# Kernel tuning notes

Hardware: AMD Instinct MI355X
Metric: run time of the kernel (lower is better)

The kernel has to match this reference:

```python
import jax, jax.numpy as jnp
import numpy as np

B, T, D_IN, D_H, F = 64, 512, 128, 512, 32


def setup_inputs() -> dict:
    key = jax.random.key(0)
    ks = jax.random.split(key, 8)
    s_in = 1.0 / np.sqrt(D_IN)
    s_h = 1.0 / np.sqrt(D_H)
    return {
        "input_sequence": jax.random.normal(ks[0], (B, T, D_IN), dtype=jnp.float32),
        "Wx0": jax.random.normal(ks[1], (D_H, D_IN), dtype=jnp.float32) * s_in,
        "b0": jnp.zeros((D_H,), dtype=jnp.float32),
        "Wh0": jax.random.normal(ks[2], (D_H, D_H), dtype=jnp.float32) * (0.8 * s_h),
        "d0": jnp.asarray(0.9, dtype=jnp.float32),
        "Wx1": jax.random.normal(ks[3], (D_H, D_H), dtype=jnp.float32) * s_h,
        "b1": jnp.zeros((D_H,), dtype=jnp.float32),
        "Wh1": jax.random.normal(ks[4], (D_H, D_H), dtype=jnp.float32) * (0.8 * s_h),
        "d1": jnp.asarray(0.9, dtype=jnp.float32),
        "Wp": jax.random.normal(ks[5], (D_IN, D_H), dtype=jnp.float32) * s_h,
        "bp": jnp.zeros((D_IN,), dtype=jnp.float32),
        "forecast_steps": F,
    }


def reference(input_sequence, Wx0, b0, Wh0, d0, Wx1, b1, Wh1, d1, Wp, bp, forecast_steps):
    batch = input_sequence.shape[0]
    hdim = Wh0.shape[0]

    def step(h0, h1, x):
        # h_t = decay * W_h h_{t-1} + W_x x_t + b ; layer 1 consumes updated h0
        h0 = d0 * (h0 @ Wh0.T) + x @ Wx0.T + b0
        h1 = d1 * (h1 @ Wh1.T) + h0 @ Wx1.T + b1
        return h0, h1

    # ---- encode context (scan over time, time-major) ----
    xs = jnp.swapaxes(input_sequence, 0, 1)  # [T, B, D_in]
    h0 = jnp.zeros((batch, hdim), dtype=input_sequence.dtype)
    h1 = jnp.zeros((batch, hdim), dtype=input_sequence.dtype)

    def enc(carry, xt):
        return step(*carry, xt), None

    (h0, h1), _ = jax.lax.scan(enc, (h0, h1), xs)

    pred0 = h1 @ Wp.T + bp  # [B, D_in]

    def dec(carry, _):
        h0, h1, p = carry
        h0, h1 = step(h0, h1, p)
        p_new = h1 @ Wp.T + bp
        return (h0, h1, p_new), p_new

    _, rest = jax.lax.scan(dec, (h0, h1, pred0), None, length=forecast_steps - 1)
    forecasts = jnp.concatenate([pred0[None], rest], axis=0)  # [F, B, D_in]
    return jnp.swapaxes(forecasts, 0, 1)  # [B, F, D_in]
```

## Files before the change

### kernel.cpp

```cpp
#include <hip/hip_runtime.h>
#include <cstddef>


typedef _Float16 f16;
typedef _Float16 f16x8 __attribute__((ext_vector_type(8)));
typedef _Float16 f16x4 __attribute__((ext_vector_type(4)));
typedef float f32x4 __attribute__((ext_vector_type(4)));

#define NCTR 32
#define LDA  136
#define ALPHAF 0.00390625f
#define RALPHAF 256.0f
#define DIN 128
#define NF 32

constexpr int SZ = 512*512;
constexpr int off_cat   = 0;
constexpr int off_catA1 = 327680;
constexpr int off_A0c   = 851968;
constexpr int off_A1c   = 1114112;
constexpr int off_Wpr   = 1376256;
constexpr int off_Wpc   = 1441792;
constexpr int off_Gr    = 1507328;
constexpr int off_Gc    = 2555904;
constexpr int off_P0    = 3604480;
constexpr int off_P1    = 5177344;
constexpr int GPr       = 6750208;
constexpr int GPc       = 7798784;
constexpr int GQr       = 8847360;
constexpr int GQc       = 9895936;
constexpr int off_Xin   = 10944512;
constexpr int BA        = 15138816;
constexpr int BB        = 17235968;
constexpr int BC        = 19333120;
constexpr int BD        = 21430272;
constexpr int off_S     = 23527424;
constexpr int off_Dc    = 25624576;
constexpr int off_Db    = 25690112;
constexpr int off_b0h   = 25952256;
constexpr int off_b1h   = 25952768;
constexpr int off_b0ah  = 25953280;
constexpr int off_b1ah  = 25953792;
constexpr int off_bph   = 25954304;
constexpr int off_bpX   = 25954432;
constexpr int off_ctr   = 25962624;

constexpr int P0r(int s){ return off_P0 + s*524288; }
constexpr int P0c(int s){ return off_P0 + s*524288 + 262144; }
constexpr int P1r(int s){ return off_P1 + s*524288; }
constexpr int P1c(int s){ return off_P1 + s*524288 + 262144; }
constexpr int Bb(int k){ return k==0 ? off_Dc : off_Db + (k-1)*65536; }

struct Op {
  int type;
  int m_off, m_rstride, rows, cols;
  int k1, x1_off, x1_ks, x1_s1, x1_s2;
  int k2, x2_off, x2_ks, x2_s1, x2_s2;
  int add_off, add_ks, add_s1, add_s2;
  int bias_off; float scale;
  int y_off, y_ks, y_s1, y_s2;
  int yt_off, yt_rstride;
  int out32, tile_base;
};
constexpr int MAXOPS = 80, MAXG = 32;
struct Plan { Op ops[MAXOPS]; int gstart[MAXG+1]; int gtiles[MAXG]; int nops, ng; };

constexpr Op mko() {
  Op o{};
  o.type=0; o.m_off=0; o.m_rstride=512; o.rows=512; o.cols=512;
  o.k1=512; o.x1_off=0; o.x1_ks=512; o.x1_s1=64; o.x1_s2=0;
  o.k2=0; o.x2_off=0; o.x2_ks=512; o.x2_s1=64; o.x2_s2=0;
  o.add_off=-1; o.add_ks=512; o.add_s1=64; o.add_s2=0;
  o.bias_off=-1; o.scale=1.0f;
  o.y_off=-1; o.y_ks=512; o.y_s1=64; o.y_s2=0;
  o.yt_off=-1; o.yt_rstride=512; o.out32=0; o.tile_base=0;
  return o;
}
constexpr int op_ntiles(const Op& o){ return (o.rows>>6)*(o.cols>>5); }

struct Builder { Plan p{}; int nops=0, ng=0, gtile=0; };
constexpr void push(Builder& b, Op o){ o.tile_base=b.gtile; b.gtile+=op_ntiles(o); b.p.ops[b.nops++]=o; }
constexpr void endg(Builder& b){ b.p.gtiles[b.ng]=b.gtile; b.ng++; b.p.gstart[b.ng]=b.nops; b.gtile=0; }

constexpr Op SQ2(int m,int mrs,int x1c,int yc,int yr){
  Op o=mko(); o.m_off=m; o.m_rstride=mrs; o.x1_off=x1c; o.y_off=yc; o.yt_off=yr; return o; }
constexpr Op SQG(int mr,int xc,int yc,int yr){
  Op o=mko(); o.rows=1024; o.cols=1024; o.k1=1024; o.m_off=mr; o.m_rstride=1024;
  o.x1_off=xc; o.x1_ks=1024; o.y_off=yc; o.y_ks=1024; o.yt_off=yr; o.yt_rstride=1024; return o; }
constexpr Op P2S(int s){
  Op o=mko(); o.cols=4096; o.bias_off=off_b0h;
  o.k2=128; o.x2_off=off_Xin; o.x2_ks=128; o.x2_s1=512; o.x2_s2=(s-1)*64;
  o.y_off=(s&1)?BA:BB;
  if (s==1){ o.m_off=off_cat+512; o.m_rstride=640; o.k1=0; }
  else { o.m_off=off_cat; o.m_rstride=640; o.k1=512; o.x1_off=(s&1)?BB:BA; }
  return o; }
constexpr Op HS(int s){
  Op o=mko(); o.m_off=off_cat; o.m_rstride=640; o.cols=4096;
  o.k1=512; o.x1_off=(s&1)?BC:BB;
  o.k2=128; o.x2_off=off_Xin; o.x2_ks=128; o.x2_s1=512; o.x2_s2=(s-1)*64;
  o.bias_off=off_b0h; o.y_off=(s&1)?BB:BC; return o; }
constexpr Op RS(int s){
  Op o=mko(); o.cols=4096; o.bias_off=off_b1h;
  if (s==1){ o.m_off=off_catA1+512; o.m_rstride=1024; o.k1=512; o.x1_off=BB; o.y_off=BD; }
  else { o.m_off=off_catA1; o.m_rstride=1024; o.k1=512; o.x1_off=(s&1)?BA:BD;
         o.k2=512; o.x2_off=(s&1)?BB:BC; o.x2_ks=512; o.x2_s1=64; o.x2_s2=0;
         o.y_off=(s&1)?BD:BA; }
  return o; }
constexpr Op SCAN(int m,int d,int inb,int outb){
  Op o=mko(); o.m_off=m; o.cols=4096-d*64; o.x1_off=inb;
  o.add_off=inb; o.add_s2=d*64; o.y_off=outb; o.y_s2=d*64; return o; }
constexpr Op SCOPY(int d,int inb,int outb){
  Op o=mko(); o.k1=0; o.cols=d*64; o.add_off=inb; o.y_off=outb; return o; }
constexpr Op FOLDL(int m,int cols,int inb,int outb){
  Op o=mko(); o.m_off=m; o.cols=cols; o.x1_off=inb; o.x1_s1=128;
  o.add_off=inb; o.add_s1=128; o.add_s2=64; o.y_off=outb; return o; }
constexpr Op DECA(int k,int moff){
  Op o=mko(); int m=1<<k;
  o.rows=1024; o.cols=m*64; o.k1=1024; o.m_off=moff; o.m_rstride=1024;
  o.x1_off=off_S; o.x1_ks=1024; o.bias_off=Bb(k);
  o.y_off=off_S; o.y_ks=1024; o.y_s2=m*64; return o; }
constexpr Op DECB(int k,int moff){
  Op o=mko(); o.rows=1024; o.cols=64; o.k1=1024; o.m_off=moff; o.m_rstride=1024;
  o.x1_off=Bb(k); o.x1_ks=1024; o.bias_off=Bb(k);
  o.y_off=Bb(k+1); o.y_ks=1024; return o; }

constexpr Plan build_plan() {
  Builder b{}; b.p.gstart[0]=0;
  push(b, SQ2(off_cat,640,off_A0c,P0c(0),P0r(0)));
  push(b, SQ2(off_catA1,1024,off_A1c,P1c(0),P1r(0)));
  { Op o=mko(); o.m_off=off_cat+512; o.m_rstride=640; o.k1=128; o.x1_off=off_Wpc; o.x1_ks=128;
    o.y_off=off_Gc+512*1024; o.y_ks=1024; o.yt_off=off_Gr+512; o.yt_rstride=1024; push(b,o); }
  { Op o=mko(); o.m_off=off_cat+512; o.m_rstride=640; o.k1=128; o.x1_off=off_bpX; o.x1_ks=128;
    o.cols=64; o.bias_off=off_b0ah; o.scale=ALPHAF; o.y_off=off_Dc; o.y_ks=1024; push(b,o); }
  push(b, P2S(1)); endg(b);
  push(b, SQ2(P0r(0),512,P0c(0),P0c(1),P0r(1)));
  push(b, SQ2(P1r(0),512,P1c(0),P1c(1),P1r(1)));
  { Op o=mko(); o.m_off=off_catA1+512; o.m_rstride=1024; o.x1_off=off_A0c;
    o.y_off=off_Gc+512; o.y_ks=1024; o.yt_off=off_Gr+512*1024; o.yt_rstride=1024; push(b,o); }
  { Op o=mko(); o.m_off=off_catA1+512; o.m_rstride=1024; o.x1_off=off_Dc; o.x1_ks=1024;
    o.cols=64; o.bias_off=off_b1ah; o.y_off=off_Dc+512; o.y_ks=1024; push(b,o); }
  push(b, P2S(2)); endg(b);
  push(b, SQ2(P0r(1),512,P0c(1),P0c(2),P0r(2)));
  push(b, SQ2(P1r(1),512,P1c(1),P1c(2),P1r(2)));
  { Op o=mko(); o.m_off=off_catA1+512; o.m_rstride=1024; o.x1_off=off_Gc+512*1024; o.x1_ks=1024;
    o.add_off=off_A1c; o.y_off=off_Gc+512*1024+512; o.y_ks=1024;
    o.yt_off=off_Gr+512*1024+512; o.yt_rstride=1024; push(b,o); }
  push(b, P2S(3)); endg(b);
  push(b, SQ2(P0r(2),512,P0c(2),P0c(0),P0r(0)));
  push(b, SQ2(P1r(2),512,P1c(2),P1c(0),P1r(0)));
  push(b, P2S(4)); endg(b);
  push(b, SQ2(P0r(0),512,P0c(0),P0c(1),P0r(1)));
  push(b, SQ2(P1r(0),512,P1c(0),P1c(1),P1r(1)));
  push(b, P2S(5)); endg(b);
  push(b, P2S(6));
  push(b, SQG(off_Gr, off_Gc, GPc, GPr)); endg(b);
  push(b, P2S(7)); endg(b);
  push(b, P2S(8)); endg(b);
  push(b, SCAN(P0r(2), 1, BB, BA)); push(b, SCOPY(1, BB, BA)); endg(b);
  push(b, SCAN(P0r(0), 2, BA, BB)); push(b, SCOPY(2, BA, BB)); endg(b);
  push(b, SCAN(P0r(1), 4, BB, BA)); push(b, SCOPY(4, BB, BA)); endg(b);
  { Op o=mko(); o.m_off=off_cat; o.m_rstride=640; o.cols=4032; o.k1=512; o.x1_off=BA;
    o.k2=128; o.x2_off=off_Xin; o.x2_ks=128; o.x2_s1=512; o.x2_s2=512;
    o.bias_off=off_b0h; o.y_off=BB; o.y_s2=64; push(b,o); }
  { Op o=mko(); o.m_off=off_cat+512; o.m_rstride=640; o.cols=64; o.k1=0;
    o.k2=128; o.x2_off=off_Xin; o.x2_ks=128; o.x2_s1=512; o.x2_s2=0;
    o.bias_off=off_b0h; o.y_off=BB; push(b,o); }
  endg(b);
  for (int s=1; s<=7; ++s){ push(b, HS(s+1)); push(b, RS(s)); endg(b); }
  push(b, RS(8));
  { Op o=mko(); o.k1=0; o.cols=64; o.add_off=BC; o.add_s2=4032; o.scale=ALPHAF;
    o.y_off=off_S; o.y_ks=1024; push(b,o); }
  endg(b);
  push(b, FOLDL(P1r(2), 2048, BA, BB)); endg(b);
  push(b, FOLDL(P1r(0), 1024, BB, BC)); endg(b);
  { Op o=mko(); o.m_off=P1r(1); o.cols=64; o.x1_off=BC; o.x1_s2=896;
    o.add_off=BC; o.add_s2=960; o.scale=ALPHAF;
    o.y_off=off_S+512; o.y_ks=1024; push(b,o); }
  endg(b);
  push(b, DECA(0, off_Gr)); push(b, DECB(0, off_Gr)); endg(b);
  push(b, DECA(1, GPr)); push(b, DECB(1, GPr)); push(b, SQG(GPr,GPc,GQc,GQr)); endg(b);
  push(b, DECA(2, GQr)); push(b, DECB(2, GQr)); push(b, SQG(GQr,GQc,GPc,GPr)); endg(b);
  push(b, DECA(3, GPr)); push(b, DECB(3, GPr)); push(b, SQG(GPr,GPc,GQc,GQr)); endg(b);
  push(b, DECA(4, GQr)); endg(b);
  { Op o=mko(); o.m_off=off_Wpr; o.rows=128; o.cols=2048; o.x1_off=off_S+512; o.x1_ks=1024;
    o.bias_off=off_bph; o.scale=RALPHAF; o.out32=1; push(b,o); }
  endg(b);
  b.p.nops=b.nops; b.p.ng=b.ng;
  return b.p;
}
static constexpr Plan h_plan = build_plan();
__device__ __constant__ Plan d_plan = h_plan;

__device__ inline void issueA4(const f16* p, f16x8 (&r)[4]) {
  asm volatile(
    "global_load_dwordx4 %0, %4, off\n\t"
    "global_load_dwordx4 %1, %4, off offset:16\n\t"
    "global_load_dwordx4 %2, %4, off offset:32\n\t"
    "global_load_dwordx4 %3, %4, off offset:48"
    : "=&v"(r[0]), "=&v"(r[1]), "=&v"(r[2]), "=&v"(r[3])
    : "v"(p) : "memory");
}
__device__ inline void issueB2(const f16* p, f16x8 (&r)[2]) {
  asm volatile(
    "global_load_dwordx4 %0, %2, off\n\t"
    "global_load_dwordx4 %1, %2, off offset:16"
    : "=&v"(r[0]), "=&v"(r[1]) : "v"(p) : "memory");
}
__device__ inline void issue_ld8(const f16* p, f16x4& r) {
  asm volatile("global_load_dwordx2 %0, %1, off"
               : "=&v"(r) : "v"(p) : "memory");
}
__device__ inline void st8_cc(f16* p, f16x4 v) {
  asm volatile("global_store_dwordx2 %0, %1, off sc0 sc1" :: "v"(p), "v"(v) : "memory");
}
__device__ inline void st2_cc(f16* p, f16 v) {
  unsigned d = __builtin_bit_cast(unsigned short, v);
  asm volatile("global_store_short %0, %1, off sc0 sc1" :: "v"(p), "v"(d) : "memory");
}
__device__ inline unsigned ld_u32_cc(const unsigned* p) {
  unsigned r;
  asm volatile("global_load_dword %0, %1, off sc0 sc1\n\ts_waitcnt vmcnt(0)"
               : "=&v"(r) : "v"(p) : "memory");
  return r;
}
__device__ inline void st_u32_cc(unsigned* p, unsigned v) {
  asm volatile("global_store_dword %0, %1, off sc0 sc1" :: "v"(p), "v"(v) : "memory");
}
__device__ inline void l2_inv() {
  asm volatile("buffer_inv sc0 sc1\n\ts_waitcnt vmcnt(0)" ::: "memory");
}

__device__ inline void grid_barrier(unsigned* ctrs, unsigned epoch) {
  __syncthreads();
  if (threadIdx.x == 0)
    __hip_atomic_fetch_add(&ctrs[(blockIdx.x & (NCTR-1))*32], 1u,
                           __ATOMIC_RELAXED, __HIP_MEMORY_SCOPE_AGENT);
  if (blockIdx.x == 0) {
    if (threadIdx.x < NCTR) {
      const unsigned tgt = epoch * (gridDim.x / NCTR);
      while (ld_u32_cc(&ctrs[threadIdx.x*32]) < tgt)
        __builtin_amdgcn_s_sleep(1);
    }
    __syncthreads();
    if (threadIdx.x < NCTR)
      st_u32_cc(&ctrs[(NCTR + threadIdx.x)*32], epoch);
  } else if (threadIdx.x == 0) {
    const unsigned fl = (NCTR + (blockIdx.x & (NCTR-1)))*32;
    while (ld_u32_cc(&ctrs[fl]) < epoch)
      __builtin_amdgcn_s_sleep(1);
  }
  if (threadIdx.x == 0) l2_inv();
  __syncthreads();
}

__device__ inline void chunk_srcs(const Op& o, const f16* w, int r0, int c0, int kc,
                                  const f16*& pa, const f16*& pb) {
  const int tid = threadIdx.x;
  pa = w + o.m_off + (size_t)(r0 + (tid>>2)) * o.m_rstride + kc + (tid&3)*32;
  int C = c0 + (tid>>3);
  int xo, xks, xs1, xs2, xk;
  if (kc < o.k1) { xo=o.x1_off; xks=o.x1_ks; xs1=o.x1_s1; xs2=o.x1_s2; xk=kc; }
  else           { xo=o.x2_off; xks=o.x2_ks; xs1=o.x2_s1; xs2=o.x2_s2; xk=kc-o.k1; }
  int xcol = xs1*(C>>6) + (C&63) + xs2;
  pb = w + xo + (size_t)xcol*xks + xk + (tid&7)*16;
}

__device__ inline void st_lds(f16* lsA, f16* lsB, const f16x8 (&ra)[4], const f16x8 (&rb)[2]) {
  const int tid = threadIdx.x;
  f16* da = lsA + (tid>>2)*LDA + (tid&3)*32;
#pragma unroll
  for (int i=0;i<4;++i) *(f16x8*)(da + i*8) = ra[i];
  f16* db = lsB + (tid>>3)*LDA + (tid&7)*16;
#pragma unroll
  for (int i=0;i<2;++i) *(f16x8*)(db + i*8) = rb[i];
}

__device__ inline void mfma_lds(const f16* lsA, const f16* lsB, f32x4 (&acc)[2]) {
  const int tid = threadIdx.x, lane = tid & 63, wid = tid >> 6;
  const int ko = (lane >> 4) * 8, rl = lane & 15;
#pragma unroll
  for (int kb = 0; kb < 4; ++kb) {
    f16x8 a = *(const f16x8*)(lsA + (wid*16 + rl) * LDA + kb*32 + ko);
#pragma unroll
    for (int n = 0; n < 2; ++n) {
      f16x8 bb = *(const f16x8*)(lsB + (n*16 + rl) * LDA + kb*32 + ko);
      acc[n] = __builtin_amdgcn_mfma_f32_16x16x32_f16(a, bb, acc[n], 0, 0, 0);
    }
  }
}

#define CH_STEP(c_, raX, rbX)                                                  \
  do {                                                                         \
    asm volatile("s_waitcnt lgkmcnt(0)" ::: "memory");                         \
    __builtin_amdgcn_s_barrier();                                              \
    __builtin_amdgcn_sched_barrier(0);                                         \
    int rem_ = nch - 1 - (c_);                                                 \
    if (rem_ >= 2)      asm volatile("s_waitcnt vmcnt(12)" ::: "memory");      \
    else if (rem_ == 1) asm volatile("s_waitcnt vmcnt(6)"  ::: "memory");      \
    else                asm volatile("s_waitcnt vmcnt(0)"  ::: "memory");      \
    __builtin_amdgcn_sched_barrier(0);                                         \
    st_lds(lsA, lsB, raX, rbX);                                                \
    asm volatile("s_waitcnt lgkmcnt(0)" ::: "memory");                         \
    __builtin_amdgcn_s_barrier();                                              \
    __builtin_amdgcn_sched_barrier(0);                                         \
    if ((c_) + 3 < nch) {                                                      \
      chunk_srcs(o, w, r0, c0, ((c_)+3)*128, pa, pb);                          \
      issueA4(pa, raX); issueB2(pb, rbX);                                      \
    }                                                                          \
    mfma_lds(lsA, lsB, acc);                                                   \
  } while (0)

__device__ void run_tile(const Op& o, int local, f16* w, float* out, f16* lsA, f16* lsB) {
  int nct = o.cols >> 5;
  int rg = local / nct, ct = local - rg * nct;
  int r0 = rg << 6, c0 = ct << 5;
  f32x4 acc[2];
  acc[0] = f32x4{0.f,0.f,0.f,0.f}; acc[1] = f32x4{0.f,0.f,0.f,0.f};
  int nch = (o.k1 + o.k2) >> 7;
  if (nch > 0) {
    const f16 *pa, *pb;
    f16x8 ra0[4], rb0[2], ra1[4], rb1[2], ra2[4], rb2[2];
    chunk_srcs(o, w, r0, c0, 0, pa, pb);
    issueA4(pa, ra0); issueB2(pb, rb0);
    if (nch > 1) { chunk_srcs(o, w, r0, c0, 128, pa, pb);
                   issueA4(pa, ra1); issueB2(pb, rb1); }
    if (nch > 2) { chunk_srcs(o, w, r0, c0, 256, pa, pb);
                   issueA4(pa, ra2); issueB2(pb, rb2); }
    for (int c = 0; c < nch; c += 3) {
      CH_STEP(c, ra0, rb0);
      if (c + 1 < nch) CH_STEP(c+1, ra1, rb1);
      if (c + 2 < nch) CH_STEP(c+2, ra2, rb2);
    }
  }
  const int tid = threadIdx.x, lane = tid & 63, wid = tid >> 6;
  const int q4 = (lane >> 4) * 4, cl = lane & 15;
  const int r = r0 + wid*16 + q4;
  f16x4 addv[2], biasv;
  bool pend = false;
  if (o.add_off >= 0) {
#pragma unroll
    for (int n = 0; n < 2; ++n) {
      int C = c0 + n*16 + cl;
      int acol = o.add_s1 * (C>>6) + (C&63) + o.add_s2;
      const f16* ap = w + o.add_off + (size_t)acol * o.add_ks + r;
      issue_ld8(ap, addv[n]); pend = true;
    }
  }
  if (o.bias_off >= 0) {
    const f16* bp2 = w + o.bias_off + r;
    issue_ld8(bp2, biasv); pend = true;
  }
  if (pend) asm volatile("s_waitcnt vmcnt(0)" ::: "memory");
#pragma unroll
  for (int n = 0; n < 2; ++n) {
    int C = c0 + n*16 + cl;
    f32x4 v = acc[n];
    if (o.add_off >= 0) {
      v[0]+=(float)addv[n][0]; v[1]+=(float)addv[n][1];
      v[2]+=(float)addv[n][2]; v[3]+=(float)addv[n][3];
    }
    v[0]*=o.scale; v[1]*=o.scale; v[2]*=o.scale; v[3]*=o.scale;
    if (o.bias_off >= 0) {
      v[0]+=(float)biasv[0]; v[1]+=(float)biasv[1];
      v[2]+=(float)biasv[2]; v[3]+=(float)biasv[3];
    }
    if (o.y_off >= 0) {
      int ycol = o.y_s1 * (C>>6) + (C&63) + o.y_s2;
      f16* yp = w + o.y_off + (size_t)ycol * o.y_ks + r;
      f16x4 h; h[0]=(f16)v[0]; h[1]=(f16)v[1]; h[2]=(f16)v[2]; h[3]=(f16)v[3];
      st8_cc(yp, h);
    }
    if (o.yt_off >= 0) {
      f16* tp = w + o.yt_off;
      st2_cc(tp + (size_t)(r+0)*o.yt_rstride + C, (f16)v[0]);
      st2_cc(tp + (size_t)(r+1)*o.yt_rstride + C, (f16)v[1]);
      st2_cc(tp + (size_t)(r+2)*o.yt_rstride + C, (f16)v[2]);
      st2_cc(tp + (size_t)(r+3)*o.yt_rstride + C, (f16)v[3]);
    }
    if (o.out32) {
      float* op2 = out + (size_t)(C & 63) * (NF*DIN) + (size_t)(C >> 6) * DIN + r;
      op2[0]=v[0]; op2[1]=v[1]; op2[2]=v[2]; op2[3]=v[3];
    }
  }
}

__global__ __launch_bounds__(256, 4) void rnn_main(f16* w, float* out) {
  __shared__ f16 lsA[64*LDA];
  __shared__ f16 lsB[32*LDA];
  unsigned* ctrs = (unsigned*)(w + off_ctr);
  const int wg = blockIdx.x;
  const int stride = gridDim.x;
  const int ng = d_plan.ng;
  for (int g = 0; g < ng; ++g) {
    int o0 = d_plan.gstart[g], o1 = d_plan.gstart[g+1];
    int gtot = d_plan.gtiles[g];
    for (int t = wg; t < gtot; t += stride) {
      int oi = o0;
      while (oi + 1 < o1 && t >= d_plan.ops[oi+1].tile_base) ++oi;
      run_tile(d_plan.ops[oi], t - d_plan.ops[oi].tile_base, w, out, lsA, lsB);
    }
    grid_barrier(ctrs, (unsigned)(g + 1));
  }
}

__global__ void rnn_prep(f16* w, const float* X, const float* Wx0, const float* b0,
    const float* Wh0, const float* d0p, const float* Wx1, const float* b1,
    const float* Wh1, const float* d1p, const float* Wp, const float* bp)
{
  const float d0 = d0p[0], d1 = d1p[0];
  const long n0=512L*640, n1=512L*1024, n2=(long)SZ, n3=(long)SZ, n4=128L*512, n5=512L*128,
             n6=(long)SZ, n7=(long)SZ, n8=32768L*128, n9=512, n10=512, n11=512, n12=512,
             n13=128, n14=64L*128, n15=2048;
  const long total = n0+n1+n2+n3+n4+n5+n6+n7+n8+n9+n10+n11+n12+n13+n14+n15;
  for (long idx = (long)blockIdx.x*blockDim.x + threadIdx.x; idx < total;
       idx += (long)gridDim.x*blockDim.x) {
    long j = idx;
    if (j < n0) { int r=(int)(j/640), c=(int)(j%640);
      w[off_cat+j] = (f16)(c<512 ? d0*Wh0[(long)r*512+c] : Wx0[(long)r*128+(c-512)]); continue; }
    j -= n0;
    if (j < n1) { int r=(int)(j>>10), c=(int)(j&1023);
      w[off_catA1+j] = (f16)(c<512 ? d1*Wh1[(long)r*512+c] : Wx1[(long)r*512+(c-512)]); continue; }
    j -= n1;
    if (j < n2) { int c=(int)(j>>9), r=(int)(j&511); w[off_A0c+j] = (f16)(d0*Wh0[(long)r*512+c]); continue; }
    j -= n2;
    if (j < n3) { int c=(int)(j>>9), r=(int)(j&511); w[off_A1c+j] = (f16)(d1*Wh1[(long)r*512+c]); continue; }
    j -= n3;
    if (j < n4) { w[off_Wpr+j] = (f16)Wp[j]; continue; }
    j -= n4;
    if (j < n5) { int c=(int)(j>>7), k=(int)(j&127); w[off_Wpc+j] = (f16)Wp[(long)k*512+c]; continue; }
    j -= n5;
    if (j < n6) { int r=(int)(j>>9), c=(int)(j&511);
      w[off_Gr + (long)r*1024 + c] = (f16)(d0*Wh0[(long)r*512+c]); continue; }
    j -= n6;
    if (j < n7) { int c=(int)(j>>9), r=(int)(j&511);
      w[off_Gc + (long)c*1024 + r] = (f16)(d0*Wh0[(long)r*512+c]); continue; }
    j -= n7;
    if (j < n8) { int col=(int)(j>>7), d=(int)(j&127); int t=col>>6, bb=col&63;
      w[off_Xin+j] = (f16)X[((long)bb<<16) + ((long)t<<7) + d]; continue; }
    j -= n8;
    if (j < n9) { w[off_b0h+j] = (f16)b0[j]; continue; }  j -= n9;
    if (j < n10){ w[off_b1h+j] = (f16)b1[j]; continue; }  j -= n10;
    if (j < n11){ w[off_b0ah+j] = (f16)(ALPHAF*b0[j]); continue; }  j -= n11;
    if (j < n12){ w[off_b1ah+j] = (f16)(ALPHAF*b1[j]); continue; }  j -= n12;
    if (j < n13){ w[off_bph+j] = (f16)bp[j]; continue; }  j -= n13;
    if (j < n14){ int k=(int)(j&127); w[off_bpX+j] = (f16)bp[k]; continue; }  j -= n14;
    ((unsigned*)(w + off_ctr))[j] = 0u;
  }
}

extern "C" void kernel_launch(void* const* d_in, const int* in_sizes, int n_in,
                              void* d_out, int out_size, void* d_ws, size_t ws_size,
                              hipStream_t stream) {
  (void)in_sizes; (void)n_in; (void)out_size; (void)ws_size;
  f16* w = (f16*)d_ws;
  hipLaunchKernelGGL(rnn_prep, dim3(2048), dim3(256), 0, stream,
      w,
      (const float*)d_in[0], (const float*)d_in[1], (const float*)d_in[2],
      (const float*)d_in[3], (const float*)d_in[4], (const float*)d_in[5],
      (const float*)d_in[6], (const float*)d_in[7], (const float*)d_in[8],
      (const float*)d_in[9], (const float*)d_in[10]);
  float* outp = (float*)d_out;
  void* kargs[] = { (void*)&w, (void*)&outp };
  int nb = 0;
  hipError_t qe = hipOccupancyMaxActiveBlocksPerMultiprocessor(
      &nb, (const void*)rnn_main, 256, 0);
  int bpc = (qe == hipSuccess && nb >= 1) ? (nb >= 4 ? 4 : (nb >= 2 ? 2 : 1)) : 1;
  int grid = 256 * bpc;
  while (true) {
    hipError_t le = hipLaunchCooperativeKernel((const void*)rnn_main, dim3(grid),
                                               dim3(256), kargs, 0, stream);
    if (le == hipSuccess || grid <= 256) break;
    grid >>= 1;
  }
}
```

Before: 607.7 us.

## Widen barrier counters, remap tiles, reuse Xin scratch, and skip final L2 invalidate

```diff
diff --git a/kernel.cpp b/kernel.cpp
--- a/kernel.cpp
+++ b/kernel.cpp
@@ -7,7 +7,7 @@
 typedef _Float16 f16x4 __attribute__((ext_vector_type(4)));
 typedef float f32x4 __attribute__((ext_vector_type(4)));
 
-#define NCTR 32
+#define NARR 128
 #define LDA  136
 #define ALPHAF 0.00390625f
 #define RALPHAF 256.0f
@@ -44,6 +44,11 @@
 constexpr int off_bph   = 25954304;
 constexpr int off_bpX   = 25954432;
 constexpr int off_ctr   = 25962624;
+
+constexpr int G8r_  = off_Xin;
+constexpr int G8c_  = off_Xin + 1048576;
+constexpr int G16r_ = off_Xin + 2097152;
+constexpr int G16c_ = off_Xin + 3145728;
 
 constexpr int P0r(int s){ return off_P0 + s*524288; }
 constexpr int P0c(int s){ return off_P0 + s*524288 + 262144; }
@@ -179,9 +184,9 @@
   endg(b);
   push(b, DECA(0, off_Gr)); push(b, DECB(0, off_Gr)); endg(b);
   push(b, DECA(1, GPr)); push(b, DECB(1, GPr)); push(b, SQG(GPr,GPc,GQc,GQr)); endg(b);
-  push(b, DECA(2, GQr)); push(b, DECB(2, GQr)); push(b, SQG(GQr,GQc,GPc,GPr)); endg(b);
-  push(b, DECA(3, GPr)); push(b, DECB(3, GPr)); push(b, SQG(GPr,GPc,GQc,GQr)); endg(b);
-  push(b, DECA(4, GQr)); endg(b);
+  push(b, DECA(2, GQr)); push(b, DECB(2, GQr)); push(b, SQG(GQr,GQc,G8c_,G8r_)); endg(b);
+  push(b, DECA(3, G8r_)); push(b, DECB(3, G8r_)); push(b, SQG(G8r_,G8c_,G16c_,G16r_)); endg(b);
+  push(b, DECA(4, G16r_)); endg(b);
   { Op o=mko(); o.m_off=off_Wpr; o.rows=128; o.cols=2048; o.x1_off=off_S+512; o.x1_ks=1024;
     o.bias_off=off_bph; o.scale=RALPHAF; o.out32=1; push(b,o); }
   endg(b);
@@ -217,6 +222,9 @@
   unsigned d = __builtin_bit_cast(unsigned short, v);
   asm volatile("global_store_short %0, %1, off sc0 sc1" :: "v"(p), "v"(d) : "memory");
 }
+__device__ inline void st16f_cc(float* p, f32x4 v) {
+  asm volatile("global_store_dwordx4 %0, %1, off sc0 sc1" :: "v"(p), "v"(v) : "memory");
+}
 __device__ inline unsigned ld_u32_cc(const unsigned* p) {
   unsigned r;
   asm volatile("global_load_dword %0, %1, off sc0 sc1\n\ts_waitcnt vmcnt(0)"
@@ -230,26 +238,26 @@
   asm volatile("buffer_inv sc0 sc1\n\ts_waitcnt vmcnt(0)" ::: "memory");
 }
 
-__device__ inline void grid_barrier(unsigned* ctrs, unsigned epoch) {
+__device__ inline void grid_barrier(unsigned* ctrs, unsigned epoch, bool inv) {
   __syncthreads();
   if (threadIdx.x == 0)
-    __hip_atomic_fetch_add(&ctrs[(blockIdx.x & (NCTR-1))*32], 1u,
+    __hip_atomic_fetch_add(&ctrs[(blockIdx.x & (NARR-1))*32], 1u,
                            __ATOMIC_RELAXED, __HIP_MEMORY_SCOPE_AGENT);
   if (blockIdx.x == 0) {
-    if (threadIdx.x < NCTR) {
-      const unsigned tgt = epoch * (gridDim.x / NCTR);
+    if (threadIdx.x < NARR) {
+      const unsigned tgt = epoch * (gridDim.x >> 7);
       while (ld_u32_cc(&ctrs[threadIdx.x*32]) < tgt)
         __builtin_amdgcn_s_sleep(1);
     }
     __syncthreads();
-    if (threadIdx.x < NCTR)
-      st_u32_cc(&ctrs[(NCTR + threadIdx.x)*32], epoch);
+    if (threadIdx.x < NARR)
+      st_u32_cc(&ctrs[(NARR + threadIdx.x)*32], epoch);
   } else if (threadIdx.x == 0) {
-    const unsigned fl = (NCTR + (blockIdx.x & (NCTR-1)))*32;
+    const unsigned fl = (NARR + (blockIdx.x & (NARR-1)))*32;
     while (ld_u32_cc(&ctrs[fl]) < epoch)
       __builtin_amdgcn_s_sleep(1);
   }
-  if (threadIdx.x == 0) l2_inv();
+  if (inv && threadIdx.x == 0) l2_inv();
   __syncthreads();
 }
 
@@ -312,7 +320,15 @@
 
 __device__ void run_tile(const Op& o, int local, f16* w, float* out, f16* lsA, f16* lsB) {
   int nct = o.cols >> 5;
-  int rg = local / nct, ct = local - rg * nct;
+  int nrt = o.rows >> 6;
+  int rg, ct;
+  if ((nct & 7) == 0) {
+    int x = local & 7, l = local >> 3, bpx = nct >> 3;
+    rg = l % nrt; int ctl = l / nrt;
+    ct = x * bpx + ctl;
+  } else {
+    rg = local / nct; ct = local - rg * nct;
+  }
   int r0 = rg << 6, c0 = ct << 5;
   f32x4 acc[2];
   acc[0] = f32x4{0.f,0.f,0.f,0.f}; acc[1] = f32x4{0.f,0.f,0.f,0.f};
@@ -379,7 +395,7 @@
     }
     if (o.out32) {
       float* op2 = out + (size_t)(C & 63) * (NF*DIN) + (size_t)(C >> 6) * DIN + r;
-      op2[0]=v[0]; op2[1]=v[1]; op2[2]=v[2]; op2[3]=v[3];
+      st16f_cc(op2, v);
     }
   }
 }
@@ -399,7 +415,7 @@
       while (oi + 1 < o1 && t >= d_plan.ops[oi+1].tile_base) ++oi;
       run_tile(d_plan.ops[oi], t - d_plan.ops[oi].tile_base, w, out, lsA, lsB);
     }
-    grid_barrier(ctrs, (unsigned)(g + 1));
+    grid_barrier(ctrs, (unsigned)(g + 1), g + 1 < ng);
   }
 }
 
@@ -410,7 +426,7 @@
   const float d0 = d0p[0], d1 = d1p[0];
   const long n0=512L*640, n1=512L*1024, n2=(long)SZ, n3=(long)SZ, n4=128L*512, n5=512L*128,
              n6=(long)SZ, n7=(long)SZ, n8=32768L*128, n9=512, n10=512, n11=512, n12=512,
-             n13=128, n14=64L*128, n15=2048;
+             n13=128, n14=64L*128, n15=8192;
   const long total = n0+n1+n2+n3+n4+n5+n6+n7+n8+n9+n10+n11+n12+n13+n14+n15;
   for (long idx = (long)blockIdx.x*blockDim.x + threadIdx.x; idx < total;
        idx += (long)gridDim.x*blockDim.x) {
```

New measurement: 605.6 us. About the same (-0.3%).
